# Optimization experiments

Hardware: AMD Instinct MI355X
Metric: run time of the kernel (lower is better)

The kernel has to match this reference:

```python
import jax, jax.numpy as jnp
import numpy as np

N = 50000      # num_nodes
E = 800000     # num_edges (avg degree 16)
D = 128        # embedding_dim
HID = 32       # per-head hidden dim of conv1
H = 8          # heads of conv1
OUT = 128      # output_dim


def setup_inputs() -> dict:
    key = jax.random.key(0)
    ks = jax.random.split(key, 14)
    s = lambda fan_in: 1.0 / np.sqrt(fan_in)
    return {
        "x": jax.random.randint(ks[0], (N,), 0, N),
        "edge_index": jax.random.randint(ks[1], (2, E), 0, N),
        "emb": jax.random.normal(ks[2], (N, D), jnp.float32),
        # conv1: GATConv(D, HID, heads=H, concat=True)
        "W1": jax.random.normal(ks[3], (D, H * HID), jnp.float32) * s(D),
        "a_src1": jax.random.normal(ks[4], (H, HID), jnp.float32) * s(HID),
        "a_dst1": jax.random.normal(ks[5], (H, HID), jnp.float32) * s(HID),
        "b1": jnp.zeros((H * HID,), jnp.float32),
        # conv2: GATConv(H*HID, OUT, heads=1, concat=False)
        "W2": jax.random.normal(ks[6], (H * HID, OUT), jnp.float32) * s(H * HID),
        "a_src2": jax.random.normal(ks[7], (1, OUT), jnp.float32) * s(OUT),
        "a_dst2": jax.random.normal(ks[8], (1, OUT), jnp.float32) * s(OUT),
        "b2": jnp.zeros((OUT,), jnp.float32),
        # output Linear(OUT, OUT)
        "Wo": jax.random.normal(ks[9], (OUT, OUT), jnp.float32) * s(OUT),
        "bo": jnp.zeros((OUT,), jnp.float32),
    }


def _segment_softmax(e, seg, n):
    # e: [E, H]; softmax over edges sharing the same destination node
    m = jax.ops.segment_max(e, seg, num_segments=n)            # [N, H]
    ex = jnp.exp(e - m[seg])
    denom = jax.ops.segment_sum(ex, seg, num_segments=n)       # [N, H]
    return ex / (denom[seg] + 1e-16)


def _gat_conv(x, src, dst, W, a_src, a_dst, b, concat):
    n = x.shape[0]
    Hh, C = a_src.shape
    h = (x @ W).reshape(n, Hh, C)                              # [N, H, C]
    al_src = (h * a_src).sum(-1)                               # [N, H]
    al_dst = (h * a_dst).sum(-1)                               # [N, H]
    e = jax.nn.leaky_relu(al_src[src] + al_dst[dst], 0.2)      # [E, H]
    alpha = _segment_softmax(e, dst, n)                        # [E, H]
    out = jax.ops.segment_sum(h[src] * alpha[:, :, None], dst, num_segments=n)
    out = out.reshape(n, Hh * C) if concat else out.mean(axis=1)
    return out + b


def reference(x, edge_index, emb, W1, a_src1, a_dst1, b1,
              W2, a_src2, a_dst2, b2, Wo, bo):
    n = x.shape[0]
    loops = jnp.arange(n)
    src = jnp.concatenate([edge_index[0], loops])              # add self-loops (PyG default)
    dst = jnp.concatenate([edge_index[1], loops])
    h = emb[x]                                                 # [N, D]
    h = _gat_conv(h, src, dst, W1, a_src1, a_dst1, b1, concat=True)
    h = _gat_conv(h, src, dst, W2, a_src2, a_dst2, b2, concat=False)
    return h @ Wo + bo
```

## Files before the change

### kernel.cpp

```cpp
#include <hip/hip_runtime.h>
#include <hip/hip_bf16.h>

#define NN 50000
#define EE 800000
#define DD 128
#define F1 256
#define F2 128

using short8  = __attribute__((ext_vector_type(8))) short;
using floatx4 = __attribute__((ext_vector_type(4))) float;

__device__ inline float bf2f(ushort u) { return __uint_as_float(((unsigned)u) << 16); }
__device__ inline ushort f2bf(float f) {
    unsigned u = __float_as_uint(f);
    u += 0x7fffu + ((u >> 16) & 1u);
    return (ushort)(u >> 16);
}

#define HB ((EE + 255) / 256)
#define GB ((NN + 1) / 2)
#define W1B ((DD * F1 + 255) / 256)
#define W2B ((F1 * F2 + 255) / 256)
#define WOB ((F2 * F2 + 255) / 256)

__global__ __launch_bounds__(256) void k_prep(
    const int* __restrict__ edst, int* __restrict__ cnt,
    const int* __restrict__ x, const float* __restrict__ emb, ushort* __restrict__ Ax,
    const float* __restrict__ W1, ushort* __restrict__ W1t,
    const float* __restrict__ W2, ushort* __restrict__ W2t,
    const float* __restrict__ Wo, ushort* __restrict__ Wot,
    const float* __restrict__ b2, const float* __restrict__ bo,
    float* __restrict__ bc) {
    int b = blockIdx.x;
    if (b < HB) {
        int i = b * 256 + threadIdx.x;
        if (i < EE) atomicAdd(&cnt[edst[i]], 1);
    } else if (b < HB + GB) {
        int row = (b - HB) * 2 + (threadIdx.x >> 7);
        if (row < NN) {
            int c = threadIdx.x & 127;
            Ax[(size_t)row * DD + c] = f2bf(emb[(size_t)x[row] * DD + c]);
        }
    } else if (b < HB + GB + W1B) {
        int idx = (b - HB - GB) * 256 + threadIdx.x;
        int k = idx / F1, n = idx % F1;
        W1t[(size_t)n * DD + k] = f2bf(W1[(size_t)k * F1 + n]);
    } else if (b < HB + GB + W1B + W2B) {
        int idx = (b - HB - GB - W1B) * 256 + threadIdx.x;
        int k = idx / F2, n = idx % F2;
        W2t[(size_t)n * F1 + k] = f2bf(W2[(size_t)k * F2 + n]);
    } else if (b < HB + GB + W1B + W2B + WOB) {
        int idx = (b - HB - GB - W1B - W2B) * 256 + threadIdx.x;
        int k = idx / F2, n = idx % F2;
        Wot[(size_t)n * F2 + k] = f2bf(Wo[(size_t)k * F2 + n]);
    } else {
        int j = threadIdx.x;
        if (j < F2) {
            float s = bo[j];
            for (int k = 0; k < F2; ++k) s += b2[k] * Wo[(size_t)k * F2 + j];
            bc[j] = s;
        }
    }
}

__global__ void k_scan1(const int* __restrict__ cnt, int* __restrict__ out,
                        int* __restrict__ sums) {
    __shared__ int s[256];
    int i = blockIdx.x * 256 + threadIdx.x;
    int v = (i < NN) ? cnt[i] + 1 : 0;
    s[threadIdx.x] = v;
    __syncthreads();
    for (int off = 1; off < 256; off <<= 1) {
        int t = (threadIdx.x >= off) ? s[threadIdx.x - off] : 0;
        __syncthreads();
        s[threadIdx.x] += t;
        __syncthreads();
    }
    if (i < NN) out[i] = s[threadIdx.x] - v;
    if (threadIdx.x == 255) sums[blockIdx.x] = s[255];
}

__global__ void k_scan3(int* __restrict__ offsets, const int* __restrict__ sums,
                        int* __restrict__ cursor, int nb) {
    __shared__ int s[256];
    int v = (threadIdx.x < nb) ? sums[threadIdx.x] : 0;
    s[threadIdx.x] = v;
    __syncthreads();
    for (int off = 1; off < 256; off <<= 1) {
        int t = (threadIdx.x >= off) ? s[threadIdx.x - off] : 0;
        __syncthreads();
        s[threadIdx.x] += t;
        __syncthreads();
    }
    int base = (blockIdx.x == 0) ? 0 : s[blockIdx.x - 1];
    int i = blockIdx.x * 256 + threadIdx.x;
    if (i < NN) {
        int o = offsets[i] + base;
        offsets[i] = o;
        cursor[i] = o;
    }
    if (blockIdx.x == 0 && threadIdx.x == 0) offsets[NN] = EE + NN;
}

__global__ void k_scatter(const int* __restrict__ esrc, const int* __restrict__ edst,
                          int* __restrict__ cursor, int* __restrict__ srcs) {
    int i = blockIdx.x * 256 + threadIdx.x;
    if (i < EE) {
        int pos = atomicAdd(&cursor[edst[i]], 1);
        srcs[pos] = esrc[i];
    } else if (i < EE + NN) {
        int n = i - EE;
        int pos = atomicAdd(&cursor[n], 1);
        srcs[pos] = n;
    }
}

template<int K, int MODE>
__global__ __launch_bounds__(256, 2) void k_mfma_gemm(
    const ushort* __restrict__ A, const ushort* __restrict__ Bt,
    void* __restrict__ Cout, int ldc, const float* __restrict__ bias,
    const float* __restrict__ avs, const float* __restrict__ avd,
    float* __restrict__ out_s, float* __restrict__ out_d) {
    __shared__ ushort As[128][72];
    __shared__ ushort Bs[128][72];
    __shared__ float als[2][128], ald[2][128];
    const int t    = threadIdx.x;
    const int lane = t & 63;
    const int w    = t >> 6;
    const int wr   = w >> 1, wc = w & 1;
    const int m0   = blockIdx.x * 128;
    const int n0   = blockIdx.y * 128;
    floatx4 acc[4][4] = {};
    for (int k0 = 0; k0 < K; k0 += 64) {
        #pragma unroll
        for (int p = 0; p < 4; ++p) {
            int linear = p * 2048 + t * 8;
            int row = linear >> 6;
            int col = linear & 63;
            short8 va = {};
            int gm = m0 + row;
            if (gm < NN) va = *(const short8*)(A + (size_t)gm * K + k0 + col);
            *(short8*)&As[row][col] = va;
            short8 vb = *(const short8*)(Bt + (size_t)(n0 + row) * K + k0 + col);
            *(short8*)&Bs[row][col] = vb;
        }
        __syncthreads();
        #pragma unroll
        for (int kk = 0; kk < 64; kk += 32) {
            const int q8 = (lane >> 4) * 8;
            short8 af[4], bf[4];
            #pragma unroll
            for (int i = 0; i < 4; ++i)
                af[i] = *(const short8*)&As[wr * 64 + i * 16 + (lane & 15)][kk + q8];
            #pragma unroll
            for (int j = 0; j < 4; ++j)
                bf[j] = *(const short8*)&Bs[wc * 64 + j * 16 + (lane & 15)][kk + q8];
            #pragma unroll
            for (int i = 0; i < 4; ++i)
                #pragma unroll
                for (int j = 0; j < 4; ++j)
                    acc[i][j] = __builtin_amdgcn_mfma_f32_16x16x32_bf16(
                        af[i], bf[j], acc[i][j], 0, 0, 0);
        }
        __syncthreads();
    }
    const int q  = lane >> 4;
    const int r0 = q * 4;
    const int cc = lane & 15;
    float as0 = 0, as1 = 0, as2 = 0, as3 = 0, ad0 = 0, ad1 = 0, ad2 = 0, ad3 = 0;
    if (MODE == 1 || MODE == 2) {
        as0 = avs[n0 + wc * 64 +  0 + cc]; ad0 = avd[n0 + wc * 64 +  0 + cc];
        as1 = avs[n0 + wc * 64 + 16 + cc]; ad1 = avd[n0 + wc * 64 + 16 + cc];
        as2 = avs[n0 + wc * 64 + 32 + cc]; ad2 = avd[n0 + wc * 64 + 32 + cc];
        as3 = avs[n0 + wc * 64 + 48 + cc]; ad3 = avd[n0 + wc * 64 + 48 + cc];
    }
    #pragma unroll
    for (int i = 0; i < 4; ++i) {
        #pragma unroll
        for (int r = 0; r < 4; ++r) {
            int m = m0 + wr * 64 + i * 16 + r0 + r;
            if (MODE == 1) {
                float hs0 = acc[i][0][r] * as0 + acc[i][1][r] * as1;
                float hs1 = acc[i][2][r] * as2 + acc[i][3][r] * as3;
                float hd0 = acc[i][0][r] * ad0 + acc[i][1][r] * ad1;
                float hd1 = acc[i][2][r] * ad2 + acc[i][3][r] * ad3;
                #pragma unroll
                for (int mask = 1; mask < 16; mask <<= 1) {
                    hs0 += __shfl_xor(hs0, mask);
                    hs1 += __shfl_xor(hs1, mask);
                    hd0 += __shfl_xor(hd0, mask);
                    hd1 += __shfl_xor(hd1, mask);
                }
                if (cc == 0 && m < NN) {
                    int gh = (n0 >> 5) + wc * 2;
                    out_s[m * 8 + gh] = hs0;   out_s[m * 8 + gh + 1] = hs1;
                    out_d[m * 8 + gh] = hd0;   out_d[m * 8 + gh + 1] = hd1;
                }
            }
            if (MODE == 2) {
                float ps = acc[i][0][r] * as0 + acc[i][1][r] * as1
                         + acc[i][2][r] * as2 + acc[i][3][r] * as3;
                float pd = acc[i][0][r] * ad0 + acc[i][1][r] * ad1
                         + acc[i][2][r] * ad2 + acc[i][3][r] * ad3;
                #pragma unroll
                for (int mask = 1; mask < 16; mask <<= 1) {
                    ps += __shfl_xor(ps, mask);
                    pd += __shfl_xor(pd, mask);
                }
                if (cc == 0) {
                    int lr = wr * 64 + i * 16 + r0 + r;
                    als[wc][lr] = ps;
                    ald[wc][lr] = pd;
                }
            }
            if (m < NN) {
                #pragma unroll
                for (int j = 0; j < 4; ++j) {
                    int n = n0 + wc * 64 + j * 16 + cc;
                    ((ushort*)Cout)[(size_t)m * ldc + n] = f2bf(acc[i][j][r]);
                }
            }
        }
    }
    if (MODE == 2) {
        __syncthreads();
        if (t < 128) {
            int m = m0 + t;
            if (m < NN) {
                out_s[m] = als[0][t] + als[1][t];
                out_d[m] = ald[0][t] + ald[1][t];
            }
        }
    }
}

__device__ inline float lrelu(float x) { return x > 0.f ? x : 0.2f * x; }

__global__ __launch_bounds__(256) void k_agg1(
    const int* __restrict__ offsets, const int* __restrict__ srcs,
    const ushort* __restrict__ h1, const float* __restrict__ a1s,
    const float* __restrict__ a1d, const float* __restrict__ b1,
    ushort* __restrict__ out1) {
    __shared__ float atab[4][1024];
    __shared__ int   stab[4][128];
    const int w = threadIdx.x >> 6;
    const int d = blockIdx.x * 4 + w;
    if (d >= NN) return;
    const int lane = threadIdx.x & 63;
    const int beg = offsets[d], end = offsets[d + 1];
    const int deg = end - beg;
    const int e8 = lane >> 3, h8 = lane & 7;
    const float ad = a1d[d * 8 + h8];
    const int hh = lane >> 3;
    float4 acc = make_float4(0.f, 0.f, 0.f, 0.f);

    if (deg <= 128) {
        float m = -1e30f, den = 0.f;
        for (int e = e8; e < deg; e += 8) {
            int s = srcs[beg + e];
            if (h8 == 0) stab[w][e] = s;
            float v = lrelu(a1s[s * 8 + h8] + ad);
            atab[w][e * 8 + h8] = v;
            float nm = fmaxf(m, v);
            den = den * __expf(m - nm) + __expf(v - nm);
            m = nm;
        }
        #pragma unroll
        for (int mask = 8; mask < 64; mask <<= 1) {
            float om = __shfl_xor(m, mask);
            float od = __shfl_xor(den, mask);
            float nm = fmaxf(m, om);
            den = den * __expf(m - nm) + od * __expf(om - nm);
            m = nm;
        }
        float rden = 1.f / (den + 1e-16f);
        for (int p = lane; p < deg * 8; p += 64)
            atab[w][p] = __expf(atab[w][p] - m) * rden;
        int e = 0;
        for (; e + 8 <= deg; e += 8) {
            ushort4 u[8]; float a[8];
            #pragma unroll
            for (int jj = 0; jj < 8; ++jj) {
                int s = stab[w][e + jj];
                u[jj] = *(const ushort4*)(h1 + (size_t)s * F1 + lane * 4);
                a[jj] = atab[w][(e + jj) * 8 + hh];
            }
            #pragma unroll
            for (int jj = 0; jj < 8; ++jj) {
                acc.x += a[jj] * bf2f(u[jj].x);
                acc.y += a[jj] * bf2f(u[jj].y);
                acc.z += a[jj] * bf2f(u[jj].z);
                acc.w += a[jj] * bf2f(u[jj].w);
            }
        }
        for (; e < deg; ++e) {
            int s = stab[w][e];
            float alpha = atab[w][e * 8 + hh];
            ushort4 u = *(const ushort4*)(h1 + (size_t)s * F1 + lane * 4);
            acc.x += alpha * bf2f(u.x); acc.y += alpha * bf2f(u.y);
            acc.z += alpha * bf2f(u.z); acc.w += alpha * bf2f(u.w);
        }
    } else {
        float m = -1e30f, den = 0.f;
        for (int i = beg + e8; i < end; i += 8) {
            int s = srcs[i];
            float v = lrelu(a1s[s * 8 + h8] + ad);
            float nm = fmaxf(m, v);
            den = den * __expf(m - nm) + __expf(v - nm);
            m = nm;
        }
        #pragma unroll
        for (int mask = 8; mask < 64; mask <<= 1) {
            float om = __shfl_xor(m, mask);
            float od = __shfl_xor(den, mask);
            float nm = fmaxf(m, om);
            den = den * __expf(m - nm) + od * __expf(om - nm);
            m = nm;
        }
        float rden = 1.f / (den + 1e-16f);
        for (int tb = beg; tb < end; tb += 64) {
            int cnt = min(64, end - tb);
            if (lane < cnt) stab[w][lane] = srcs[tb + lane];
            int np = cnt * 8;
            for (int p = lane; p < np; p += 64) {
                int s = stab[w][p >> 3];
                float v = lrelu(a1s[s * 8 + h8] + ad);
                atab[w][p] = __expf(v - m) * rden;
            }
            for (int e = 0; e < cnt; ++e) {
                int s = stab[w][e];
                float alpha = atab[w][e * 8 + hh];
                ushort4 u = *(const ushort4*)(h1 + (size_t)s * F1 + lane * 4);
                acc.x += alpha * bf2f(u.x); acc.y += alpha * bf2f(u.y);
                acc.z += alpha * bf2f(u.z); acc.w += alpha * bf2f(u.w);
            }
        }
    }
    float4 bb = *(const float4*)(b1 + lane * 4);
    ushort4 o;
    o.x = f2bf(acc.x + bb.x); o.y = f2bf(acc.y + bb.y);
    o.z = f2bf(acc.z + bb.z); o.w = f2bf(acc.w + bb.w);
    *(ushort4*)(out1 + (size_t)d * F1 + lane * 4) = o;
}

__global__ __launch_bounds__(256) void k_agg2(
    const int* __restrict__ offsets, const int* __restrict__ srcs,
    const ushort* __restrict__ h3, const float* __restrict__ a2s,
    const float* __restrict__ a2d, const float* __restrict__ bc,
    float* __restrict__ out) {
    __shared__ float atab[4][128];
    __shared__ int   stab[4][128];
    const int w = threadIdx.x >> 6;
    const int d = blockIdx.x * 4 + w;
    if (d >= NN) return;
    const int lane = threadIdx.x & 63;
    const int beg = offsets[d], end = offsets[d + 1];
    const int deg = end - beg;
    const float ad = a2d[d];
    float2 acc = make_float2(0.f, 0.f);

    if (deg <= 128) {
        float m = -1e30f, den = 0.f;
        for (int e = lane; e < deg; e += 64) {
            int s = srcs[beg + e];
            stab[w][e] = s;
            float v = lrelu(a2s[s] + ad);
            atab[w][e] = v;
            float nm = fmaxf(m, v);
            den = den * __expf(m - nm) + __expf(v - nm);
            m = nm;
        }
        #pragma unroll
        for (int mask = 1; mask < 64; mask <<= 1) {
            float om = __shfl_xor(m, mask);
            float od = __shfl_xor(den, mask);
            float nm = fmaxf(m, om);
            den = den * __expf(m - nm) + od * __expf(om - nm);
            m = nm;
        }
        float rden = 1.f / (den + 1e-16f);
        for (int p = lane; p < deg; p += 64)
            atab[w][p] = __expf(atab[w][p] - m) * rden;
        int e = 0;
        for (; e + 8 <= deg; e += 8) {
            ushort2 u[8]; float a[8];
            #pragma unroll
            for (int jj = 0; jj < 8; ++jj) {
                int s = stab[w][e + jj];
                u[jj] = *(const ushort2*)(h3 + (size_t)s * F2 + lane * 2);
                a[jj] = atab[w][e + jj];
            }
            #pragma unroll
            for (int jj = 0; jj < 8; ++jj) {
                acc.x += a[jj] * bf2f(u[jj].x);
                acc.y += a[jj] * bf2f(u[jj].y);
            }
        }
        for (; e < deg; ++e) {
            int s = stab[w][e];
            float alpha = atab[w][e];
            ushort2 u = *(const ushort2*)(h3 + (size_t)s * F2 + lane * 2);
            acc.x += alpha * bf2f(u.x); acc.y += alpha * bf2f(u.y);
        }
    } else {
        float m = -1e30f, den = 0.f;
        for (int i = beg + lane; i < end; i += 64) {
            int s = srcs[i];
            float v = lrelu(a2s[s] + ad);
            float nm = fmaxf(m, v);
            den = den * __expf(m - nm) + __expf(v - nm);
            m = nm;
        }
        #pragma unroll
        for (int mask = 1; mask < 64; mask <<= 1) {
            float om = __shfl_xor(m, mask);
            float od = __shfl_xor(den, mask);
            float nm = fmaxf(m, om);
            den = den * __expf(m - nm) + od * __expf(om - nm);
            m = nm;
        }
        float rden = 1.f / (den + 1e-16f);
        for (int tb = beg; tb < end; tb += 64) {
            int cnt = min(64, end - tb);
            if (lane < cnt) {
                int s = srcs[tb + lane];
                stab[w][lane] = s;
                atab[w][lane] = __expf(lrelu(a2s[s] + ad) - m) * rden;
            }
            for (int e = 0; e < cnt; ++e) {
                int s = stab[w][e];
                float alpha = atab[w][e];
                ushort2 u = *(const ushort2*)(h3 + (size_t)s * F2 + lane * 2);
                acc.x += alpha * bf2f(u.x); acc.y += alpha * bf2f(u.y);
            }
        }
    }
    float2 bb = *(const float2*)(bc + lane * 2);
    *(float2*)(out + (size_t)d * F2 + lane * 2) = make_float2(acc.x + bb.x, acc.y + bb.y);
}

extern "C" void kernel_launch(void* const* d_in, const int* in_sizes, int n_in,
                              void* d_out, int out_size, void* d_ws, size_t ws_size,
                              hipStream_t stream) {
    const int*   x      = (const int*)d_in[0];
    const int*   edge   = (const int*)d_in[1];
    const float* emb    = (const float*)d_in[2];
    const float* W1     = (const float*)d_in[3];
    const float* a_src1 = (const float*)d_in[4];
    const float* a_dst1 = (const float*)d_in[5];
    const float* b1     = (const float*)d_in[6];
    const float* W2     = (const float*)d_in[7];
    const float* a_src2 = (const float*)d_in[8];
    const float* a_dst2 = (const float*)d_in[9];
    const float* b2     = (const float*)d_in[10];
    const float* Wo     = (const float*)d_in[11];
    const float* bo     = (const float*)d_in[12];
    float* out = (float*)d_out;

    char* w = (char*)d_ws;
    auto alloc = [&](size_t bytes) {
        char* p = w;
        w += (bytes + 255) & ~(size_t)255;
        return p;
    };
    int*    offsets = (int*)alloc((NN + 1) * sizeof(int));
    int*    cursor  = (int*)alloc(NN * sizeof(int));
    int*    sums    = (int*)alloc(256 * sizeof(int));
    int*    srcs    = (int*)alloc((size_t)(EE + NN) * sizeof(int));
    ushort* Ax      = (ushort*)alloc((size_t)NN * DD * sizeof(ushort));
    ushort* W1t     = (ushort*)alloc((size_t)DD * F1 * sizeof(ushort));
    ushort* W2t     = (ushort*)alloc((size_t)F1 * F2 * sizeof(ushort));
    ushort* Wot     = (ushort*)alloc((size_t)F2 * F2 * sizeof(ushort));
    ushort* h1      = (ushort*)alloc((size_t)NN * F1 * sizeof(ushort));
    ushort* out1    = (ushort*)alloc((size_t)NN * F1 * sizeof(ushort));
    ushort* h2      = (ushort*)alloc((size_t)NN * F2 * sizeof(ushort));
    ushort* h3      = (ushort*)alloc((size_t)NN * F2 * sizeof(ushort));
    float*  a1s     = (float*)alloc((size_t)NN * 8 * sizeof(float));
    float*  a1d     = (float*)alloc((size_t)NN * 8 * sizeof(float));
    float*  bc      = (float*)alloc(F2 * sizeof(float));
    float*  a2s     = a1s;
    float*  a2d     = a1d;

    const int* esrc = edge;
    const int* edst = edge + EE;

    const int NB = (NN + 255) / 256;

    hipMemsetAsync(cursor, 0, NN * sizeof(int), stream);
    k_prep<<<HB + GB + W1B + W2B + WOB + 1, 256, 0, stream>>>(
        edst, cursor, x, emb, Ax, W1, W1t, W2, W2t, Wo, Wot, b2, bo, bc);
    k_scan1<<<NB, 256, 0, stream>>>(cursor, offsets, sums);
    k_scan3<<<NB, 256, 0, stream>>>(offsets, sums, cursor, NB);
    k_scatter<<<(EE + NN + 255) / 256, 256, 0, stream>>>(esrc, edst, cursor, srcs);

    const int MT = (NN + 127) / 128;

    k_mfma_gemm<DD, 1><<<dim3(MT, F1 / 128), 256, 0, stream>>>(
        Ax, W1t, h1, F1, nullptr, a_src1, a_dst1, a1s, a1d);
    k_agg1<<<(NN + 3) / 4, 256, 0, stream>>>(offsets, srcs, h1, a1s, a1d, b1, out1);

    k_mfma_gemm<F1, 2><<<dim3(MT, 1), 256, 0, stream>>>(
        out1, W2t, h2, F2, nullptr, a_src2, a_dst2, a2s, a2d);

    k_mfma_gemm<F2, 0><<<dim3(MT, 1), 256, 0, stream>>>(
        h2, Wot, h3, F2, nullptr, nullptr, nullptr, nullptr, nullptr);

    k_agg2<<<(NN + 3) / 4, 256, 0, stream>>>(offsets, srcs, h3, a2s, a2d, bc, out);
}
```

Baseline: 364.2 us.

## Fuse conv2 GEMM with output Linear GEMM and shrink aggregation shared buffers

The conv2 projection GEMM and the output Linear GEMM now run in one kernel. The h2 tile is written to shared memory in bf16 and multiplied by Wo directly, so the h2 round trip through global memory and one kernel launch go away. The aggregation kernels also cut their shared-memory tables from 128 to 64 edges, and agg2 handles the softmax stats with a single lane-per-edge pass, so nodes with degree above 64 now take the fallback path. The fused kernel needs about 68KB of LDS, which may lower occupancy.

```diff
diff --git a/kernel.cpp b/kernel.cpp
--- a/kernel.cpp
+++ b/kernel.cpp
@@ -115,15 +115,13 @@
     }
 }
 
-template<int K, int MODE>
-__global__ __launch_bounds__(256, 2) void k_mfma_gemm(
+__global__ __launch_bounds__(256, 2) void k_gemm1(
     const ushort* __restrict__ A, const ushort* __restrict__ Bt,
-    void* __restrict__ Cout, int ldc, const float* __restrict__ bias,
+    ushort* __restrict__ Cout,
     const float* __restrict__ avs, const float* __restrict__ avd,
     float* __restrict__ out_s, float* __restrict__ out_d) {
     __shared__ ushort As[128][72];
     __shared__ ushort Bs[128][72];
-    __shared__ float als[2][128], ald[2][128];
     const int t    = threadIdx.x;
     const int lane = t & 63;
     const int w    = t >> 6;
@@ -131,7 +129,7 @@
     const int m0   = blockIdx.x * 128;
     const int n0   = blockIdx.y * 128;
     floatx4 acc[4][4] = {};
-    for (int k0 = 0; k0 < K; k0 += 64) {
+    for (int k0 = 0; k0 < DD; k0 += 64) {
         #pragma unroll
         for (int p = 0; p < 4; ++p) {
             int linear = p * 2048 + t * 8;
@@ -139,9 +137,9 @@
             int col = linear & 63;
             short8 va = {};
             int gm = m0 + row;
-            if (gm < NN) va = *(const short8*)(A + (size_t)gm * K + k0 + col);
+            if (gm < NN) va = *(const short8*)(A + (size_t)gm * DD + k0 + col);
             *(short8*)&As[row][col] = va;
-            short8 vb = *(const short8*)(Bt + (size_t)(n0 + row) * K + k0 + col);
+            short8 vb = *(const short8*)(Bt + (size_t)(n0 + row) * DD + k0 + col);
             *(short8*)&Bs[row][col] = vb;
         }
         __syncthreads();
@@ -164,40 +162,105 @@
         }
         __syncthreads();
     }
-    const int q  = lane >> 4;
-    const int r0 = q * 4;
+    const int r0 = (lane >> 4) * 4;
     const int cc = lane & 15;
-    float as0 = 0, as1 = 0, as2 = 0, as3 = 0, ad0 = 0, ad1 = 0, ad2 = 0, ad3 = 0;
-    if (MODE == 1 || MODE == 2) {
-        as0 = avs[n0 + wc * 64 +  0 + cc]; ad0 = avd[n0 + wc * 64 +  0 + cc];
-        as1 = avs[n0 + wc * 64 + 16 + cc]; ad1 = avd[n0 + wc * 64 + 16 + cc];
-        as2 = avs[n0 + wc * 64 + 32 + cc]; ad2 = avd[n0 + wc * 64 + 32 + cc];
-        as3 = avs[n0 + wc * 64 + 48 + cc]; ad3 = avd[n0 + wc * 64 + 48 + cc];
-    }
+    float as0 = avs[n0 + wc * 64 +  0 + cc], ad0 = avd[n0 + wc * 64 +  0 + cc];
+    float as1 = avs[n0 + wc * 64 + 16 + cc], ad1 = avd[n0 + wc * 64 + 16 + cc];
+    float as2 = avs[n0 + wc * 64 + 32 + cc], ad2 = avd[n0 + wc * 64 + 32 + cc];
+    float as3 = avs[n0 + wc * 64 + 48 + cc], ad3 = avd[n0 + wc * 64 + 48 + cc];
     #pragma unroll
     for (int i = 0; i < 4; ++i) {
         #pragma unroll
         for (int r = 0; r < 4; ++r) {
             int m = m0 + wr * 64 + i * 16 + r0 + r;
-            if (MODE == 1) {
-                float hs0 = acc[i][0][r] * as0 + acc[i][1][r] * as1;
-                float hs1 = acc[i][2][r] * as2 + acc[i][3][r] * as3;
-                float hd0 = acc[i][0][r] * ad0 + acc[i][1][r] * ad1;
-                float hd1 = acc[i][2][r] * ad2 + acc[i][3][r] * ad3;
+            float hs0 = acc[i][0][r] * as0 + acc[i][1][r] * as1;
+            float hs1 = acc[i][2][r] * as2 + acc[i][3][r] * as3;
+            float hd0 = acc[i][0][r] * ad0 + acc[i][1][r] * ad1;
+            float hd1 = acc[i][2][r] * ad2 + acc[i][3][r] * ad3;
+            #pragma unroll
+            for (int mask = 1; mask < 16; mask <<= 1) {
+                hs0 += __shfl_xor(hs0, mask);
+                hs1 += __shfl_xor(hs1, mask);
+                hd0 += __shfl_xor(hd0, mask);
+                hd1 += __shfl_xor(hd1, mask);
+            }
+            if (cc == 0 && m < NN) {
+                int gh = (n0 >> 5) + wc * 2;
+                out_s[m * 8 + gh] = hs0;   out_s[m * 8 + gh + 1] = hs1;
+                out_d[m * 8 + gh] = hd0;   out_d[m * 8 + gh + 1] = hd1;
+            }
+            if (m < NN) {
                 #pragma unroll
-                for (int mask = 1; mask < 16; mask <<= 1) {
-                    hs0 += __shfl_xor(hs0, mask);
-                    hs1 += __shfl_xor(hs1, mask);
-                    hd0 += __shfl_xor(hd0, mask);
-                    hd1 += __shfl_xor(hd1, mask);
-                }
-                if (cc == 0 && m < NN) {
-                    int gh = (n0 >> 5) + wc * 2;
-                    out_s[m * 8 + gh] = hs0;   out_s[m * 8 + gh + 1] = hs1;
-                    out_d[m * 8 + gh] = hd0;   out_d[m * 8 + gh + 1] = hd1;
-                }
-            }
-            if (MODE == 2) {
+                for (int j = 0; j < 4; ++j)
+                    Cout[(size_t)m * F1 + n0 + wc * 64 + j * 16 + cc] = f2bf(acc[i][j][r]);
+            }
+        }
+    }
+}
+
+__global__ __launch_bounds__(256, 2) void k_gemm23(
+    const ushort* __restrict__ A,
+    const ushort* __restrict__ Bt,
+    const ushort* __restrict__ Wot,
+    ushort* __restrict__ h3,
+    const float* __restrict__ avs, const float* __restrict__ avd,
+    float* __restrict__ out_s, float* __restrict__ out_d) {
+    __shared__ __align__(16) char smem[69632];
+    ushort (*As)[72]   = (ushort(*)[72])smem;
+    ushort (*Bs)[72]   = (ushort(*)[72])(smem + 18432);
+    ushort (*h2t)[136] = (ushort(*)[136])smem;
+    ushort (*Wt)[136]  = (ushort(*)[136])(smem + 34816);
+    __shared__ float als[2][128], ald[2][128];
+    const int t    = threadIdx.x;
+    const int lane = t & 63;
+    const int w    = t >> 6;
+    const int wr   = w >> 1, wc = w & 1;
+    const int m0   = blockIdx.x * 128;
+    floatx4 acc[4][4] = {};
+    for (int k0 = 0; k0 < F1; k0 += 64) {
+        #pragma unroll
+        for (int p = 0; p < 4; ++p) {
+            int linear = p * 2048 + t * 8;
+            int row = linear >> 6;
+            int col = linear & 63;
+            short8 va = {};
+            int gm = m0 + row;
+            if (gm < NN) va = *(const short8*)(A + (size_t)gm * F1 + k0 + col);
+            *(short8*)&As[row][col] = va;
+            short8 vb = *(const short8*)(Bt + (size_t)row * F1 + k0 + col);
+            *(short8*)&Bs[row][col] = vb;
+        }
+        __syncthreads();
+        #pragma unroll
+        for (int kk = 0; kk < 64; kk += 32) {
+            const int q8 = (lane >> 4) * 8;
+            short8 af[4], bf[4];
+            #pragma unroll
+            for (int i = 0; i < 4; ++i)
+                af[i] = *(const short8*)&As[wr * 64 + i * 16 + (lane & 15)][kk + q8];
+            #pragma unroll
+            for (int j = 0; j < 4; ++j)
+                bf[j] = *(const short8*)&Bs[wc * 64 + j * 16 + (lane & 15)][kk + q8];
+            #pragma unroll
+            for (int i = 0; i < 4; ++i)
+                #pragma unroll
+                for (int j = 0; j < 4; ++j)
+                    acc[i][j] = __builtin_amdgcn_mfma_f32_16x16x32_bf16(
+                        af[i], bf[j], acc[i][j], 0, 0, 0);
+        }
+        __syncthreads();
+    }
+    const int r0 = (lane >> 4) * 4;
+    const int cc = lane & 15;
+    {
+        float as0 = avs[wc * 64 +  0 + cc], ad0 = avd[wc * 64 +  0 + cc];
+        float as1 = avs[wc * 64 + 16 + cc], ad1 = avd[wc * 64 + 16 + cc];
+        float as2 = avs[wc * 64 + 32 + cc], ad2 = avd[wc * 64 + 32 + cc];
+        float as3 = avs[wc * 64 + 48 + cc], ad3 = avd[wc * 64 + 48 + cc];
+        #pragma unroll
+        for (int i = 0; i < 4; ++i) {
+            #pragma unroll
+            for (int r = 0; r < 4; ++r) {
                 float ps = acc[i][0][r] * as0 + acc[i][1][r] * as1
                          + acc[i][2][r] * as2 + acc[i][3][r] * as3;
                 float pd = acc[i][0][r] * ad0 + acc[i][1][r] * ad1
@@ -213,22 +276,57 @@
                     ald[wc][lr] = pd;
                 }
             }
+        }
+    }
+    #pragma unroll
+    for (int i = 0; i < 4; ++i)
+        #pragma unroll
+        for (int r = 0; r < 4; ++r)
+            #pragma unroll
+            for (int j = 0; j < 4; ++j)
+                h2t[wr * 64 + i * 16 + r0 + r][wc * 64 + j * 16 + cc] = f2bf(acc[i][j][r]);
+    #pragma unroll
+    for (int p = 0; p < 8; ++p) {
+        int linear = p * 2048 + t * 8;
+        int row = linear >> 7;
+        int col = linear & 127;
+        *(short8*)&Wt[row][col] = *(const short8*)(Wot + (size_t)row * F2 + col);
+    }
+    __syncthreads();
+    if (t < 128) {
+        int m = m0 + t;
+        if (m < NN) {
+            out_s[m] = als[0][t] + als[1][t];
+            out_d[m] = ald[0][t] + ald[1][t];
+        }
+    }
+    floatx4 acc2[4][4] = {};
+    #pragma unroll
+    for (int kk = 0; kk < 128; kk += 32) {
+        const int q8 = (lane >> 4) * 8;
+        short8 af[4], bf[4];
+        #pragma unroll
+        for (int i = 0; i < 4; ++i)
+            af[i] = *(const short8*)&h2t[wr * 64 + i * 16 + (lane & 15)][kk + q8];
+        #pragma unroll
+        for (int j = 0; j < 4; ++j)
+            bf[j] = *(const short8*)&Wt[wc * 64 + j * 16 + (lane & 15)][kk + q8];
+        #pragma unroll
+        for (int i = 0; i < 4; ++i)
+            #pragma unroll
+            for (int j = 0; j < 4; ++j)
+                acc2[i][j] = __builtin_amdgcn_mfma_f32_16x16x32_bf16(
+                    af[i], bf[j], acc2[i][j], 0, 0, 0);
+    }
+    #pragma unroll
+    for (int i = 0; i < 4; ++i) {
+        #pragma unroll
+        for (int r = 0; r < 4; ++r) {
+            int m = m0 + wr * 64 + i * 16 + r0 + r;
             if (m < NN) {
                 #pragma unroll
-                for (int j = 0; j < 4; ++j) {
-                    int n = n0 + wc * 64 + j * 16 + cc;
-                    ((ushort*)Cout)[(size_t)m * ldc + n] = f2bf(acc[i][j][r]);
-                }
-            }
-        }
-    }
-    if (MODE == 2) {
-        __syncthreads();
-        if (t < 128) {
-            int m = m0 + t;
-            if (m < NN) {
-                out_s[m] = als[0][t] + als[1][t];
-                out_d[m] = ald[0][t] + ald[1][t];
+                for (int j = 0; j < 4; ++j)
+                    h3[(size_t)m * F2 + wc * 64 + j * 16 + cc] = f2bf(acc2[i][j][r]);
             }
         }
     }
@@ -241,8 +339,8 @@
     const ushort* __restrict__ h1, const float* __restrict__ a1s,
     const float* __restrict__ a1d, const float* __restrict__ b1,
     ushort* __restrict__ out1) {
-    __shared__ float atab[4][1024];
-    __shared__ int   stab[4][128];
+    __shared__ float atab[4][512];
+    __shared__ int   stab[4][64];
     const int w = threadIdx.x >> 6;
     const int d = blockIdx.x * 4 + w;
     if (d >= NN) return;
@@ -254,7 +352,7 @@
     const int hh = lane >> 3;
     float4 acc = make_float4(0.f, 0.f, 0.f, 0.f);
 
-    if (deg <= 128) {
+    if (deg <= 64) {
         float m = -1e30f, den = 0.f;
         for (int e = e8; e < deg; e += 8) {
             int s = srcs[beg + e];
@@ -348,8 +446,8 @@
     const ushort* __restrict__ h3, const float* __restrict__ a2s,
     const float* __restrict__ a2d, const float* __restrict__ bc,
     float* __restrict__ out) {
-    __shared__ float atab[4][128];
-    __shared__ int   stab[4][128];
+    __shared__ float atab[4][64];
+    __shared__ int   stab[4][64];
     const int w = threadIdx.x >> 6;
     const int d = blockIdx.x * 4 + w;
     if (d >= NN) return;
@@ -359,16 +457,15 @@
     const float ad = a2d[d];
     float2 acc = make_float2(0.f, 0.f);
 
-    if (deg <= 128) {
+    if (deg <= 64) {
         float m = -1e30f, den = 0.f;
-        for (int e = lane; e < deg; e += 64) {
-            int s = srcs[beg + e];
-            stab[w][e] = s;
+        if (lane < deg) {
+            int s = srcs[beg + lane];
+            stab[w][lane] = s;
             float v = lrelu(a2s[s] + ad);
-            atab[w][e] = v;
-            float nm = fmaxf(m, v);
-            den = den * __expf(m - nm) + __expf(v - nm);
-            m = nm;
+            atab[w][lane] = v;
+            m = v;
+            den = 1.f;
         }
         #pragma unroll
         for (int mask = 1; mask < 64; mask <<= 1) {
@@ -379,8 +476,8 @@
             m = nm;
         }
         float rden = 1.f / (den + 1e-16f);
-        for (int p = lane; p < deg; p += 64)
-            atab[w][p] = __expf(atab[w][p] - m) * rden;
+        if (lane < deg)
+            atab[w][lane] = __expf(atab[w][lane] - m) * rden;
         int e = 0;
         for (; e + 8 <= deg; e += 8) {
             ushort2 u[8]; float a[8];
@@ -473,7 +570,6 @@
     ushort* Wot     = (ushort*)alloc((size_t)F2 * F2 * sizeof(ushort));
     ushort* h1      = (ushort*)alloc((size_t)NN * F1 * sizeof(ushort));
     ushort* out1    = (ushort*)alloc((size_t)NN * F1 * sizeof(ushort));
-    ushort* h2      = (ushort*)alloc((size_t)NN * F2 * sizeof(ushort));
     ushort* h3      = (ushort*)alloc((size_t)NN * F2 * sizeof(ushort));
     float*  a1s     = (float*)alloc((size_t)NN * 8 * sizeof(float));
     float*  a1d     = (float*)alloc((size_t)NN * 8 * sizeof(float));
@@ -495,15 +591,12 @@
 
     const int MT = (NN + 127) / 128;
 
-    k_mfma_gemm<DD, 1><<<dim3(MT, F1 / 128), 256, 0, stream>>>(
-        Ax, W1t, h1, F1, nullptr, a_src1, a_dst1, a1s, a1d);
+    k_gemm1<<<dim3(MT, F1 / 128), 256, 0, stream>>>(
+        Ax, W1t, h1, a_src1, a_dst1, a1s, a1d);
     k_agg1<<<(NN + 3) / 4, 256, 0, stream>>>(offsets, srcs, h1, a1s, a1d, b1, out1);
 
-    k_mfma_gemm<F1, 2><<<dim3(MT, 1), 256, 0, stream>>>(
-        out1, W2t, h2, F2, nullptr, a_src2, a_dst2, a2s, a2d);
-
-    k_mfma_gemm<F2, 0><<<dim3(MT, 1), 256, 0, stream>>>(
-        h2, Wot, h3, F2, nullptr, nullptr, nullptr, nullptr, nullptr);
+    k_gemm23<<<dim3(MT, 1), 256, 0, stream>>>(
+        out1, W2t, Wot, h3, a_src2, a_dst2, a2s, a2d);
 
     k_agg2<<<(NN + 3) / 4, 256, 0, stream>>>(offsets, srcs, h3, a2s, a2d, bc, out);
 }
```

Result: no change. 357.6 us (-1.8%).
